# Performance work log

Measured on AMD Instinct MI355X. Metric: run time of the kernel, lower is better.

The kernel has to match this reference:

```python
import jax, jax.numpy as jnp
import numpy as np

B, N, D, H = 4, 1024, 1024, 8
HD = D // H  # head dim = 128


def _layernorm(x, g, b, eps=1e-5):
    mu = jnp.mean(x, axis=-1, keepdims=True)
    var = jnp.mean(jnp.square(x - mu), axis=-1, keepdims=True)
    return (x - mu) * jax.lax.rsqrt(var + eps) * g + b


def setup_inputs() -> dict:
    key = jax.random.key(0)
    ks = jax.random.split(key, 8)
    x = jax.random.normal(ks[0], (B, N, D), dtype=jnp.float32)
    adj = (jax.random.uniform(ks[1], (B, N, N)) < 0.02).astype(jnp.int32)
    adj = jnp.maximum(adj, jnp.eye(N, dtype=jnp.int32)[None])  # self-loops: no empty softmax rows
    stoich = jax.random.normal(ks[2], (B, N), dtype=jnp.float32)
    s = 0.02
    W1 = jax.random.normal(ks[3], (D, 4 * D), dtype=jnp.float32) * s
    W2 = jax.random.normal(ks[4], (4 * D, D), dtype=jnp.float32) * s
    gW = jax.random.normal(ks[5], (D,), dtype=jnp.float32) * s  # Linear(1, D) weight
    return {
        "x": x, "adj_matrix": adj, "stoichiometry": stoich,
        "ln1_g": jnp.ones((D,), jnp.float32), "ln1_b": jnp.zeros((D,), jnp.float32),
        "ln2_g": jnp.ones((D,), jnp.float32), "ln2_b": jnp.zeros((D,), jnp.float32),
        "W1": W1, "b1": jnp.zeros((4 * D,), jnp.float32),
        "W2": W2, "b2": jnp.zeros((D,), jnp.float32),
        "gW": gW, "gb": jnp.zeros((D,), jnp.float32),
    }


def reference(x, adj_matrix, stoichiometry, ln1_g, ln1_b, ln2_g, ln2_b, W1, b1, W2, b2, gW, gb):
    normed = _layernorm(x, ln1_g, ln1_b)
    # q = k = v = normed, split into heads: [B, H, N, HD]
    qkv = normed.reshape(B, N, H, HD).transpose(0, 2, 1, 3)
    scores = jnp.einsum("bhqd,bhkd->bhqk", qkv, qkv) / jnp.sqrt(jnp.float32(HD))
    # stoichiometry gate: Linear(1, D) + sigmoid -> [B, N, D]; broadcast as [B, 1, N, D] (D == N)
    gates = jax.nn.sigmoid(stoichiometry[:, :, None] * gW + gb)[:, None]  # [B,1,N,N]
    mask = adj_matrix[:, None] > 0  # [B,1,N,N]
    # gate only valid entries (equivalent to (-inf)*gate since gate>0), then mask
    masked = jnp.where(mask, scores * gates, -jnp.inf)
    attn = jax.nn.softmax(masked, axis=-1)
    out = jnp.einsum("bhqk,bhkd->bhqd", attn, qkv)
    out = out.transpose(0, 2, 1, 3).reshape(B, N, D)
    x = x + out
    normed2 = _layernorm(x, ln2_g, ln2_b)
    mlp = jax.nn.gelu(normed2 @ W1 + b1, approximate=False) @ W2 + b2
    return x + mlp
```

## Files before the change

### kernel.cpp

```cpp
#include <hip/hip_runtime.h>
#include <math.h>

#define NTOK 1024
#define DMODEL 1024
#define NHEAD 8
#define HDIM 128
#define BATCH 4

typedef __bf16 bf16x8 __attribute__((ext_vector_type(8)));
typedef float  f32x4  __attribute__((ext_vector_type(4)));
typedef unsigned short ushort_t;

static __device__ __forceinline__ ushort_t f2bf(float f) {
  unsigned u = __float_as_uint(f);
  u += 0x7fffu + ((u >> 16) & 1u);
  return (ushort_t)(u >> 16);
}

static __device__ __forceinline__ float fast_gelu(float v) {
  const float u = 1.5957691216057308f * (v + 0.044715f * v * v * v);
  return v / (1.f + __expf(-u));
}

static __device__ __forceinline__ void gld16(void* lds, const void* g) {
  __builtin_amdgcn_global_load_lds(
      (const __attribute__((address_space(1))) void*)g,
      (__attribute__((address_space(3))) void*)lds, 16, 0, 0);
}

__global__ __launch_bounds__(256) void ln_kernel(
    const float* __restrict__ x, const float* __restrict__ g,
    const float* __restrict__ b, float* __restrict__ out)
{
  const int row = blockIdx.x;
  const int tid = threadIdx.x;
  const float* xr = x + (size_t)row * DMODEL;
  float4 v = *(const float4*)(xr + 4 * tid);
  float s1 = v.x + v.y + v.z + v.w;
  float s2 = v.x * v.x + v.y * v.y + v.z * v.z + v.w * v.w;
#pragma unroll
  for (int d = 1; d < 64; d <<= 1) { s1 += __shfl_xor(s1, d); s2 += __shfl_xor(s2, d); }
  __shared__ float red[10];
  const int wid = tid >> 6;
  if ((tid & 63) == 0) { red[wid] = s1; red[4 + wid] = s2; }
  __syncthreads();
  if (tid == 0) {
    float a = red[0] + red[1] + red[2] + red[3];
    float c = red[4] + red[5] + red[6] + red[7];
    float mu = a / (float)DMODEL;
    float var = c / (float)DMODEL - mu * mu;
    red[8] = mu; red[9] = rsqrtf(var + 1e-5f);
  }
  __syncthreads();
  const float mu = red[8], inv = red[9];
  float4 gg = *(const float4*)(g + 4 * tid);
  float4 bb = *(const float4*)(b + 4 * tid);
  float4 o;
  o.x = (v.x - mu) * inv * gg.x + bb.x;
  o.y = (v.y - mu) * inv * gg.y + bb.y;
  o.z = (v.z - mu) * inv * gg.z + bb.z;
  o.w = (v.w - mu) * inv * gg.w + bb.w;
  *(float4*)(out + (size_t)row * DMODEL + 4 * tid) = o;
}

__global__ __launch_bounds__(256) void attn_kernel(
    const float* __restrict__ x, const float* __restrict__ normed,
    const int* __restrict__ adj, const float* __restrict__ stoich,
    const float* __restrict__ gW, const float* __restrict__ gb,
    const float* __restrict__ ln2g, const float* __restrict__ ln2b,
    const float* __restrict__ b2,
    float* __restrict__ outbase, ushort_t* __restrict__ normed2)
{
  __shared__ int   neigh[NTOK];
  __shared__ float gateS[NTOK];
  __shared__ int   cntS;
  __shared__ float red[10];

  const int bq = blockIdx.x;
  const int b = bq >> 10, q = bq & 1023;
  const int tid = threadIdx.x;

  if (tid == 0) cntS = 0;
  __syncthreads();
  const int* arow = adj + ((size_t)b * NTOK + q) * NTOK;
  {
    const int4 a4 = ((const int4*)arow)[tid];
    const int k0 = 4 * tid;
    if (a4.x > 0) { int p = atomicAdd(&cntS, 1); neigh[p] = k0; }
    if (a4.y > 0) { int p = atomicAdd(&cntS, 1); neigh[p] = k0 + 1; }
    if (a4.z > 0) { int p = atomicAdd(&cntS, 1); neigh[p] = k0 + 2; }
    if (a4.w > 0) { int p = atomicAdd(&cntS, 1); neigh[p] = k0 + 3; }
  }
  __syncthreads();
  const int cnt = cntS;

  const float st = stoich[b * NTOK + q];
  for (int i = tid; i < cnt; i += 256) {
    int k = neigh[i];
    float z = fmaf(st, gW[k], gb[k]);
    gateS[i] = 1.f / (1.f + __expf(-z));
  }
  __syncthreads();

  const float* nb = normed + (size_t)b * NTOK * DMODEL;
  const float4 qv = *(const float4*)(nb + (size_t)q * DMODEL + 4 * tid);
  const float scale = 0.08838834764831845f;

  float lsum = 0.f;
  float4 o = make_float4(0.f, 0.f, 0.f, 0.f);

  for (int i0 = 0; i0 < cnt; i0 += 8) {
    float4 kv[8]; float w8[8];
#pragma unroll
    for (int u = 0; u < 8; ++u) {
      const int i = i0 + u;
      const int ii = (i < cnt) ? i : 0;
      kv[u] = *(const float4*)(nb + (size_t)neigh[ii] * DMODEL + 4 * tid);
      w8[u] = gateS[ii];
    }
#pragma unroll
    for (int u = 0; u < 8; ++u) {
      float p = kv[u].x * qv.x + kv[u].y * qv.y + kv[u].z * qv.z + kv[u].w * qv.w;
      p += __shfl_xor(p, 1);  p += __shfl_xor(p, 2);  p += __shfl_xor(p, 4);
      p += __shfl_xor(p, 8);  p += __shfl_xor(p, 16);
      w8[u] *= p * scale;
    }
#pragma unroll
    for (int u = 0; u < 8; ++u)
      w8[u] = (i0 + u < cnt) ? __expf(w8[u]) : 0.f;
#pragma unroll
    for (int u = 0; u < 8; ++u) {
      lsum += w8[u];
      o.x = fmaf(w8[u], kv[u].x, o.x);
      o.y = fmaf(w8[u], kv[u].y, o.y);
      o.z = fmaf(w8[u], kv[u].z, o.z);
      o.w = fmaf(w8[u], kv[u].w, o.w);
    }
  }
  const float pinv = 1.f / lsum;

  const float4 xv = *(const float4*)(x + ((size_t)b * NTOK + q) * DMODEL + 4 * tid);
  float4 r;
  r.x = xv.x + o.x * pinv; r.y = xv.y + o.y * pinv;
  r.z = xv.z + o.z * pinv; r.w = xv.w + o.w * pinv;

  const float4 b2v = *(const float4*)(b2 + 4 * tid);
  float4 ob;
  ob.x = r.x + b2v.x; ob.y = r.y + b2v.y;
  ob.z = r.z + b2v.z; ob.w = r.w + b2v.w;
  *(float4*)(outbase + ((size_t)b * NTOK + q) * DMODEL + 4 * tid) = ob;

  float s1 = r.x + r.y + r.z + r.w;
  float s2 = r.x * r.x + r.y * r.y + r.z * r.z + r.w * r.w;
#pragma unroll
  for (int d = 1; d < 64; d <<= 1) { s1 += __shfl_xor(s1, d); s2 += __shfl_xor(s2, d); }
  const int wid = tid >> 6;
  if ((tid & 63) == 0) { red[wid] = s1; red[4 + wid] = s2; }
  __syncthreads();
  if (tid == 0) {
    float a = red[0] + red[1] + red[2] + red[3];
    float c = red[4] + red[5] + red[6] + red[7];
    float mu = a / (float)DMODEL;
    float var = c / (float)DMODEL - mu * mu;
    red[8] = mu; red[9] = rsqrtf(var + 1e-5f);
  }
  __syncthreads();
  const float mu = red[8], inv = red[9];
  float4 gg = *(const float4*)(ln2g + 4 * tid);
  float4 bb = *(const float4*)(ln2b + 4 * tid);
  ushort4 pk;
  pk.x = f2bf((r.x - mu) * inv * gg.x + bb.x);
  pk.y = f2bf((r.y - mu) * inv * gg.y + bb.y);
  pk.z = f2bf((r.z - mu) * inv * gg.z + bb.z);
  pk.w = f2bf((r.w - mu) * inv * gg.w + bb.w);
  *(ushort4*)(normed2 + ((size_t)b * NTOK + q) * DMODEL + 4 * tid) = pk;
}

__global__ __launch_bounds__(256) void transpose_bf16(
    const float* __restrict__ W, ushort_t* __restrict__ Wt, int K, int N)
{
  __shared__ float t[32][33];
  const int kb = blockIdx.y * 32, nb = blockIdx.x * 32;
  const int c = threadIdx.x & 31, r0 = threadIdx.x >> 5;
#pragma unroll
  for (int r = r0; r < 32; r += 8)
    t[r][c] = W[(size_t)(kb + r) * N + nb + c];
  __syncthreads();
#pragma unroll
  for (int r = r0; r < 32; r += 8)
    Wt[(size_t)(nb + r) * K + kb + c] = f2bf(t[c][r]);
}

__global__ __launch_bounds__(256) void gemm_mfma_gelu(
    const ushort_t* __restrict__ A, const ushort_t* __restrict__ Bt,
    const float* __restrict__ bias, ushort_t* __restrict__ Cout,
    int M, int N, int K)
{
  __shared__ __align__(16) ushort_t As[128 * 32];
  __shared__ __align__(16) ushort_t Bs[128 * 32];

  const int tid = threadIdx.x;
  const int w = tid >> 6, l = tid & 63;
  const int bm = blockIdx.y * 128, bn = blockIdx.x * 128;
  const int wm = (w >> 1) * 64, wn = (w & 1) * 64;

  const int srow = tid >> 2;
  const int kelem = (tid & 3) * 8;
  const ushort_t* Ag0 = A + (size_t)(bm + srow) * K + kelem;
  const ushort_t* Ag1 = A + (size_t)(bm + srow + 64) * K + kelem;
  const ushort_t* Bg0 = Bt + (size_t)(bn + srow) * K + kelem;
  const ushort_t* Bg1 = Bt + (size_t)(bn + srow + 64) * K + kelem;
  ushort_t* AsW0 = As + w * 512;
  ushort_t* AsW1 = As + w * 512 + 2048;
  ushort_t* BsW0 = Bs + w * 512;
  ushort_t* BsW1 = Bs + w * 512 + 2048;

  const int quad = l >> 4, lrow = l & 15;
  const ushort_t* aRd = As + (wm + lrow) * 32 + quad * 8;
  const ushort_t* bRd = Bs + (wn + lrow) * 32 + quad * 8;

  f32x4 acc[4][4] = {};

  for (int kb = 0; kb < K; kb += 32) {
    __syncthreads();
    gld16(AsW0, Ag0 + kb);
    gld16(AsW1, Ag1 + kb);
    gld16(BsW0, Bg0 + kb);
    gld16(BsW1, Bg1 + kb);
    __syncthreads();
    bf16x8 af[4], bfr[4];
#pragma unroll
    for (int i = 0; i < 4; ++i) af[i] = *(const bf16x8*)(aRd + i * 16 * 32);
#pragma unroll
    for (int j = 0; j < 4; ++j) bfr[j] = *(const bf16x8*)(bRd + j * 16 * 32);
#pragma unroll
    for (int i = 0; i < 4; ++i)
#pragma unroll
      for (int j = 0; j < 4; ++j)
        acc[i][j] = __builtin_amdgcn_mfma_f32_16x16x32_bf16(af[i], bfr[j], acc[i][j], 0, 0, 0);
  }

#pragma unroll
  for (int i = 0; i < 4; ++i) {
    const int row0 = bm + wm + 16 * i + quad * 4;
#pragma unroll
    for (int j = 0; j < 4; ++j) {
      const int col = bn + wn + 16 * j + lrow;
      const float bi = bias[col];
#pragma unroll
      for (int r = 0; r < 4; ++r) {
        const int row = row0 + r;
        Cout[(size_t)row * N + col] = f2bf(fast_gelu(acc[i][j][r] + bi));
      }
    }
  }
}

__global__ __launch_bounds__(256) void gemm_mfma_splitk(
    const ushort_t* __restrict__ A, const ushort_t* __restrict__ Bt,
    float* __restrict__ Cout, int M, int N, int K, int kchunk)
{
  __shared__ __align__(16) ushort_t As[128 * 32];
  __shared__ __align__(16) ushort_t Bs[128 * 32];

  const int tid = threadIdx.x;
  const int w = tid >> 6, l = tid & 63;
  const int bm = blockIdx.y * 128, bn = blockIdx.x * 128;
  const int wm = (w >> 1) * 64, wn = (w & 1) * 64;
  const int koff = blockIdx.z * kchunk;

  const int srow = tid >> 2;
  const int kelem = (tid & 3) * 8;
  const ushort_t* Ag0 = A + (size_t)(bm + srow) * K + koff + kelem;
  const ushort_t* Ag1 = A + (size_t)(bm + srow + 64) * K + koff + kelem;
  const ushort_t* Bg0 = Bt + (size_t)(bn + srow) * K + koff + kelem;
  const ushort_t* Bg1 = Bt + (size_t)(bn + srow + 64) * K + koff + kelem;
  ushort_t* AsW0 = As + w * 512;
  ushort_t* AsW1 = As + w * 512 + 2048;
  ushort_t* BsW0 = Bs + w * 512;
  ushort_t* BsW1 = Bs + w * 512 + 2048;

  const int quad = l >> 4, lrow = l & 15;
  const ushort_t* aRd = As + (wm + lrow) * 32 + quad * 8;
  const ushort_t* bRd = Bs + (wn + lrow) * 32 + quad * 8;

  f32x4 acc[4][4] = {};

  for (int kb = 0; kb < kchunk; kb += 32) {
    __syncthreads();
    gld16(AsW0, Ag0 + kb);
    gld16(AsW1, Ag1 + kb);
    gld16(BsW0, Bg0 + kb);
    gld16(BsW1, Bg1 + kb);
    __syncthreads();
    bf16x8 af[4], bfr[4];
#pragma unroll
    for (int i = 0; i < 4; ++i) af[i] = *(const bf16x8*)(aRd + i * 16 * 32);
#pragma unroll
    for (int j = 0; j < 4; ++j) bfr[j] = *(const bf16x8*)(bRd + j * 16 * 32);
#pragma unroll
    for (int i = 0; i < 4; ++i)
#pragma unroll
      for (int j = 0; j < 4; ++j)
        acc[i][j] = __builtin_amdgcn_mfma_f32_16x16x32_bf16(af[i], bfr[j], acc[i][j], 0, 0, 0);
  }

#pragma unroll
  for (int i = 0; i < 4; ++i) {
    const int row0 = bm + wm + 16 * i + quad * 4;
#pragma unroll
    for (int j = 0; j < 4; ++j) {
      const int col = bn + wn + 16 * j + lrow;
#pragma unroll
      for (int r = 0; r < 4; ++r) {
        const int row = row0 + r;
        atomicAdd(&Cout[(size_t)row * N + col], acc[i][j][r]);
      }
    }
  }
}

extern "C" void kernel_launch(void* const* d_in, const int* in_sizes, int n_in,
                              void* d_out, int out_size, void* d_ws, size_t ws_size,
                              hipStream_t stream) {
  const float* x      = (const float*)d_in[0];
  const int*   adj    = (const int*)d_in[1];
  const float* stoich = (const float*)d_in[2];
  const float* ln1g   = (const float*)d_in[3];
  const float* ln1b   = (const float*)d_in[4];
  const float* ln2g   = (const float*)d_in[5];
  const float* ln2b   = (const float*)d_in[6];
  const float* W1     = (const float*)d_in[7];
  const float* b1     = (const float*)d_in[8];
  const float* W2     = (const float*)d_in[9];
  const float* b2     = (const float*)d_in[10];
  const float* gW     = (const float*)d_in[11];
  const float* gb     = (const float*)d_in[12];
  float* out = (float*)d_out;
  char* ws = (char*)d_ws;

  float*    normed  = (float*)(ws);
  ushort_t* normed2 = (ushort_t*)(ws + (16u << 20));
  ushort_t* hidden  = (ushort_t*)(ws + (24u << 20));
  ushort_t* W1t     = (ushort_t*)(ws + (56u << 20));
  ushort_t* W2t     = (ushort_t*)(ws + (64u << 20));

  const int ROWS = BATCH * NTOK;

  transpose_bf16<<<dim3(4096 / 32, 1024 / 32), 256, 0, stream>>>(W1, W1t, 1024, 4096);
  transpose_bf16<<<dim3(1024 / 32, 4096 / 32), 256, 0, stream>>>(W2, W2t, 4096, 1024);

  ln_kernel<<<ROWS, 256, 0, stream>>>(x, ln1g, ln1b, normed);
  attn_kernel<<<ROWS, 256, 0, stream>>>(x, normed, adj, stoich, gW, gb,
                                        ln2g, ln2b, b2, out, normed2);
  gemm_mfma_gelu<<<dim3(32, 32), 256, 0, stream>>>(normed2, W1t, b1, hidden,
                                                   ROWS, 4096, 1024);
  gemm_mfma_splitk<<<dim3(8, 32, 2), 256, 0, stream>>>(hidden, W2t, out,
                                                       ROWS, 1024, 4096, 2048);
}
```

Baseline: 302.3 us.

## Store LN1 output as bf16 and process two query rows per attention block

The first layernorm now writes its output in bf16 instead of fp32. The attention kernel gathers neighbour rows as 8-wide bf16 vectors, which halves the bytes read per gathered key/value row. Each 256-thread block now handles two query rows, with 128 threads per row and 8 dims per thread, so each block does more work and issues wider loads. This adds bf16 rounding to the q/k/v values, which slightly changes attention accuracy.

```diff
diff --git a/kernel.cpp b/kernel.cpp
--- a/kernel.cpp
+++ b/kernel.cpp
@@ -10,12 +10,16 @@
 typedef __bf16 bf16x8 __attribute__((ext_vector_type(8)));
 typedef float  f32x4  __attribute__((ext_vector_type(4)));
 typedef unsigned short ushort_t;
+typedef unsigned short us8 __attribute__((ext_vector_type(8)));
 
 static __device__ __forceinline__ ushort_t f2bf(float f) {
   unsigned u = __float_as_uint(f);
   u += 0x7fffu + ((u >> 16) & 1u);
   return (ushort_t)(u >> 16);
 }
+static __device__ __forceinline__ float bf2f(ushort_t v) {
+  return __uint_as_float(((unsigned)v) << 16);
+}
 
 static __device__ __forceinline__ float fast_gelu(float v) {
   const float u = 1.5957691216057308f * (v + 0.044715f * v * v * v);
@@ -30,7 +34,7 @@
 
 __global__ __launch_bounds__(256) void ln_kernel(
     const float* __restrict__ x, const float* __restrict__ g,
-    const float* __restrict__ b, float* __restrict__ out)
+    const float* __restrict__ b, ushort_t* __restrict__ out)
 {
   const int row = blockIdx.x;
   const int tid = threadIdx.x;
@@ -55,74 +59,87 @@
   const float mu = red[8], inv = red[9];
   float4 gg = *(const float4*)(g + 4 * tid);
   float4 bb = *(const float4*)(b + 4 * tid);
-  float4 o;
-  o.x = (v.x - mu) * inv * gg.x + bb.x;
-  o.y = (v.y - mu) * inv * gg.y + bb.y;
-  o.z = (v.z - mu) * inv * gg.z + bb.z;
-  o.w = (v.w - mu) * inv * gg.w + bb.w;
-  *(float4*)(out + (size_t)row * DMODEL + 4 * tid) = o;
+  ushort4 o;
+  o.x = f2bf((v.x - mu) * inv * gg.x + bb.x);
+  o.y = f2bf((v.y - mu) * inv * gg.y + bb.y);
+  o.z = f2bf((v.z - mu) * inv * gg.z + bb.z);
+  o.w = f2bf((v.w - mu) * inv * gg.w + bb.w);
+  *(ushort4*)(out + (size_t)row * DMODEL + 4 * tid) = o;
 }
 
 __global__ __launch_bounds__(256) void attn_kernel(
-    const float* __restrict__ x, const float* __restrict__ normed,
+    const float* __restrict__ x, const ushort_t* __restrict__ normedB,
     const int* __restrict__ adj, const float* __restrict__ stoich,
     const float* __restrict__ gW, const float* __restrict__ gb,
     const float* __restrict__ ln2g, const float* __restrict__ ln2b,
     const float* __restrict__ b2,
     float* __restrict__ outbase, ushort_t* __restrict__ normed2)
 {
-  __shared__ int   neigh[NTOK];
-  __shared__ float gateS[NTOK];
-  __shared__ int   cntS;
-  __shared__ float red[10];
-
-  const int bq = blockIdx.x;
-  const int b = bq >> 10, q = bq & 1023;
+  __shared__ int   neigh[2][NTOK];
+  __shared__ float gateS[2][NTOK];
+  __shared__ int   cntS[2];
+  __shared__ float red[2][6];
+
   const int tid = threadIdx.x;
-
-  if (tid == 0) cntS = 0;
-  __syncthreads();
-  const int* arow = adj + ((size_t)b * NTOK + q) * NTOK;
+  const int sub = tid >> 7;
+  const int t   = tid & 127;
+  const int row = blockIdx.x * 2 + sub;
+  const int b   = row >> 10;
+
+  if (tid < 2) cntS[tid] = 0;
+  __syncthreads();
+  const int* arow = adj + (size_t)row * NTOK;
   {
-    const int4 a4 = ((const int4*)arow)[tid];
-    const int k0 = 4 * tid;
-    if (a4.x > 0) { int p = atomicAdd(&cntS, 1); neigh[p] = k0; }
-    if (a4.y > 0) { int p = atomicAdd(&cntS, 1); neigh[p] = k0 + 1; }
-    if (a4.z > 0) { int p = atomicAdd(&cntS, 1); neigh[p] = k0 + 2; }
-    if (a4.w > 0) { int p = atomicAdd(&cntS, 1); neigh[p] = k0 + 3; }
-  }
-  __syncthreads();
-  const int cnt = cntS;
-
-  const float st = stoich[b * NTOK + q];
-  for (int i = tid; i < cnt; i += 256) {
-    int k = neigh[i];
-    float z = fmaf(st, gW[k], gb[k]);
-    gateS[i] = 1.f / (1.f + __expf(-z));
-  }
-  __syncthreads();
-
-  const float* nb = normed + (size_t)b * NTOK * DMODEL;
-  const float4 qv = *(const float4*)(nb + (size_t)q * DMODEL + 4 * tid);
+    int4 a4 = ((const int4*)arow)[t];
+    int k0 = 4 * t;
+    if (a4.x > 0) { int p = atomicAdd(&cntS[sub], 1); neigh[sub][p] = k0; }
+    if (a4.y > 0) { int p = atomicAdd(&cntS[sub], 1); neigh[sub][p] = k0 + 1; }
+    if (a4.z > 0) { int p = atomicAdd(&cntS[sub], 1); neigh[sub][p] = k0 + 2; }
+    if (a4.w > 0) { int p = atomicAdd(&cntS[sub], 1); neigh[sub][p] = k0 + 3; }
+    a4 = ((const int4*)arow)[t + 128];
+    k0 = 4 * (t + 128);
+    if (a4.x > 0) { int p = atomicAdd(&cntS[sub], 1); neigh[sub][p] = k0; }
+    if (a4.y > 0) { int p = atomicAdd(&cntS[sub], 1); neigh[sub][p] = k0 + 1; }
+    if (a4.z > 0) { int p = atomicAdd(&cntS[sub], 1); neigh[sub][p] = k0 + 2; }
+    if (a4.w > 0) { int p = atomicAdd(&cntS[sub], 1); neigh[sub][p] = k0 + 3; }
+  }
+  __syncthreads();
+  const int cnt = cntS[sub];
+
+  const float st = stoich[row];
+  for (int i = t; i < cnt; i += 128) {
+    int k = neigh[sub][i];
+    gateS[sub][i] = 1.f / (1.f + __expf(-fmaf(st, gW[k], gb[k])));
+  }
+  __syncthreads();
+
+  const ushort_t* nbB = normedB + (size_t)b * NTOK * DMODEL;
+  const int d0 = 8 * t;
+  us8 qu = *(const us8*)(nbB + (size_t)(row & 1023) * DMODEL + d0);
+  float qv[8];
+#pragma unroll
+  for (int j = 0; j < 8; ++j) qv[j] = bf2f(qu[j]);
   const float scale = 0.08838834764831845f;
 
   float lsum = 0.f;
-  float4 o = make_float4(0.f, 0.f, 0.f, 0.f);
+  float o[8] = {0.f, 0.f, 0.f, 0.f, 0.f, 0.f, 0.f, 0.f};
 
   for (int i0 = 0; i0 < cnt; i0 += 8) {
-    float4 kv[8]; float w8[8];
+    us8 ku[8]; float w8[8];
 #pragma unroll
     for (int u = 0; u < 8; ++u) {
       const int i = i0 + u;
       const int ii = (i < cnt) ? i : 0;
-      kv[u] = *(const float4*)(nb + (size_t)neigh[ii] * DMODEL + 4 * tid);
-      w8[u] = gateS[ii];
+      ku[u] = *(const us8*)(nbB + (size_t)neigh[sub][ii] * DMODEL + d0);
+      w8[u] = gateS[sub][ii];
     }
 #pragma unroll
     for (int u = 0; u < 8; ++u) {
-      float p = kv[u].x * qv.x + kv[u].y * qv.y + kv[u].z * qv.z + kv[u].w * qv.w;
-      p += __shfl_xor(p, 1);  p += __shfl_xor(p, 2);  p += __shfl_xor(p, 4);
-      p += __shfl_xor(p, 8);  p += __shfl_xor(p, 16);
+      float p = 0.f;
+#pragma unroll
+      for (int j = 0; j < 8; ++j) p = fmaf(bf2f(ku[u][j]), qv[j], p);
+      p += __shfl_xor(p, 1); p += __shfl_xor(p, 2);
+      p += __shfl_xor(p, 4); p += __shfl_xor(p, 8);
       w8[u] *= p * scale;
     }
 #pragma unroll
@@ -131,49 +148,57 @@
 #pragma unroll
     for (int u = 0; u < 8; ++u) {
       lsum += w8[u];
-      o.x = fmaf(w8[u], kv[u].x, o.x);
-      o.y = fmaf(w8[u], kv[u].y, o.y);
-      o.z = fmaf(w8[u], kv[u].z, o.z);
-      o.w = fmaf(w8[u], kv[u].w, o.w);
+#pragma unroll
+      for (int j = 0; j < 8; ++j) o[j] = fmaf(w8[u], bf2f(ku[u][j]), o[j]);
     }
   }
   const float pinv = 1.f / lsum;
 
-  const float4 xv = *(const float4*)(x + ((size_t)b * NTOK + q) * DMODEL + 4 * tid);
-  float4 r;
-  r.x = xv.x + o.x * pinv; r.y = xv.y + o.y * pinv;
-  r.z = xv.z + o.z * pinv; r.w = xv.w + o.w * pinv;
-
-  const float4 b2v = *(const float4*)(b2 + 4 * tid);
-  float4 ob;
-  ob.x = r.x + b2v.x; ob.y = r.y + b2v.y;
-  ob.z = r.z + b2v.z; ob.w = r.w + b2v.w;
-  *(float4*)(outbase + ((size_t)b * NTOK + q) * DMODEL + 4 * tid) = ob;
-
-  float s1 = r.x + r.y + r.z + r.w;
-  float s2 = r.x * r.x + r.y * r.y + r.z * r.z + r.w * r.w;
+  const float* xr = x + (size_t)row * DMODEL + d0;
+  const float4 xa = *(const float4*)(xr);
+  const float4 xb = *(const float4*)(xr + 4);
+  float r[8];
+  r[0] = xa.x + o[0] * pinv; r[1] = xa.y + o[1] * pinv;
+  r[2] = xa.z + o[2] * pinv; r[3] = xa.w + o[3] * pinv;
+  r[4] = xb.x + o[4] * pinv; r[5] = xb.y + o[5] * pinv;
+  r[6] = xb.z + o[6] * pinv; r[7] = xb.w + o[7] * pinv;
+
+  const float4 ba = *(const float4*)(b2 + d0);
+  const float4 bbv = *(const float4*)(b2 + d0 + 4);
+  float4 oa, ob;
+  oa.x = r[0] + ba.x;  oa.y = r[1] + ba.y;  oa.z = r[2] + ba.z;  oa.w = r[3] + ba.w;
+  ob.x = r[4] + bbv.x; ob.y = r[5] + bbv.y; ob.z = r[6] + bbv.z; ob.w = r[7] + bbv.w;
+  float* obp = outbase + (size_t)row * DMODEL + d0;
+  *(float4*)(obp) = oa;
+  *(float4*)(obp + 4) = ob;
+
+  float s1 = 0.f, s2 = 0.f;
+#pragma unroll
+  for (int j = 0; j < 8; ++j) { s1 += r[j]; s2 += r[j] * r[j]; }
 #pragma unroll
   for (int d = 1; d < 64; d <<= 1) { s1 += __shfl_xor(s1, d); s2 += __shfl_xor(s2, d); }
-  const int wid = tid >> 6;
-  if ((tid & 63) == 0) { red[wid] = s1; red[4 + wid] = s2; }
-  __syncthreads();
-  if (tid == 0) {
-    float a = red[0] + red[1] + red[2] + red[3];
-    float c = red[4] + red[5] + red[6] + red[7];
+  const int wsub = (tid >> 6) & 1;
+  if ((tid & 63) == 0) { red[sub][wsub] = s1; red[sub][2 + wsub] = s2; }
+  __syncthreads();
+  if ((tid & 127) == 0) {
+    float a = red[sub][0] + red[sub][1];
+    float c = red[sub][2] + red[sub][3];
     float mu = a / (float)DMODEL;
     float var = c / (float)DMODEL - mu * mu;
-    red[8] = mu; red[9] = rsqrtf(var + 1e-5f);
-  }
-  __syncthreads();
-  const float mu = red[8], inv = red[9];
-  float4 gg = *(const float4*)(ln2g + 4 * tid);
-  float4 bb = *(const float4*)(ln2b + 4 * tid);
-  ushort4 pk;
-  pk.x = f2bf((r.x - mu) * inv * gg.x + bb.x);
-  pk.y = f2bf((r.y - mu) * inv * gg.y + bb.y);
-  pk.z = f2bf((r.z - mu) * inv * gg.z + bb.z);
-  pk.w = f2bf((r.w - mu) * inv * gg.w + bb.w);
-  *(ushort4*)(normed2 + ((size_t)b * NTOK + q) * DMODEL + 4 * tid) = pk;
+    red[sub][4] = mu; red[sub][5] = rsqrtf(var + 1e-5f);
+  }
+  __syncthreads();
+  const float mu = red[sub][4], inv = red[sub][5];
+  const float4 ga = *(const float4*)(ln2g + d0);
+  const float4 gbv = *(const float4*)(ln2g + d0 + 4);
+  const float4 la = *(const float4*)(ln2b + d0);
+  const float4 lb = *(const float4*)(ln2b + d0 + 4);
+  const float gg[8] = {ga.x, ga.y, ga.z, ga.w, gbv.x, gbv.y, gbv.z, gbv.w};
+  const float ll[8] = {la.x, la.y, la.z, la.w, lb.x, lb.y, lb.z, lb.w};
+  us8 pk;
+#pragma unroll
+  for (int j = 0; j < 8; ++j) pk[j] = f2bf((r[j] - mu) * inv * gg[j] + ll[j]);
+  *(us8*)(normed2 + (size_t)row * DMODEL + d0) = pk;
 }
 
 __global__ __launch_bounds__(256) void transpose_bf16(
@@ -339,7 +364,7 @@
   float* out = (float*)d_out;
   char* ws = (char*)d_ws;
 
-  float*    normed  = (float*)(ws);
+  ushort_t* normedB = (ushort_t*)(ws);
   ushort_t* normed2 = (ushort_t*)(ws + (16u << 20));
   ushort_t* hidden  = (ushort_t*)(ws + (24u << 20));
   ushort_t* W1t     = (ushort_t*)(ws + (56u << 20));
@@ -350,9 +375,9 @@
   transpose_bf16<<<dim3(4096 / 32, 1024 / 32), 256, 0, stream>>>(W1, W1t, 1024, 4096);
   transpose_bf16<<<dim3(1024 / 32, 4096 / 32), 256, 0, stream>>>(W2, W2t, 4096, 1024);
 
-  ln_kernel<<<ROWS, 256, 0, stream>>>(x, ln1g, ln1b, normed);
-  attn_kernel<<<ROWS, 256, 0, stream>>>(x, normed, adj, stoich, gW, gb,
-                                        ln2g, ln2b, b2, out, normed2);
+  ln_kernel<<<ROWS, 256, 0, stream>>>(x, ln1g, ln1b, normedB);
+  attn_kernel<<<ROWS / 2, 256, 0, stream>>>(x, normedB, adj, stoich, gW, gb,
+                                            ln2g, ln2b, b2, out, normed2);
   gemm_mfma_gelu<<<dim3(32, 32), 256, 0, stream>>>(normed2, W1t, b1, hidden,
                                                    ROWS, 4096, 1024);
   gemm_mfma_splitk<<<dim3(8, 32, 2), 256, 0, stream>>>(hidden, W2t, out,
```

After: 295.2 us. 2.4% less time.
